# Kernel tuning notes

Hardware: AMD Instinct MI355X
Metric: run time of the kernel (lower is better)

The kernel has to match this reference:

```python
import jax, jax.numpy as jnp
import numpy as np

NP_, NT_, D_, E_, EP_, L_, R_ = 100000, 300000, 64, 2000000, 500000, 2, 2


def setup_inputs() -> dict:
    key = jax.random.key(0)
    ks = jax.random.split(key, 12)
    return {
        "emb_playlist": jax.random.normal(ks[0], (NP_, D_), jnp.float32),
        "emb_track": jax.random.normal(ks[1], (NT_, D_), jnp.float32),
        "W_rel": jax.random.normal(ks[2], (L_, R_, D_, D_), jnp.float32) * 0.1,
        "W_root": jax.random.normal(ks[3], (L_, D_, D_), jnp.float32) * 0.1,
        "bias": jnp.zeros((L_, D_), jnp.float32),
        "n_id_playlist": jnp.arange(NP_, dtype=jnp.int32),
        "n_id_track": jnp.arange(NT_, dtype=jnp.int32),
        "edge_pt_src": jax.random.randint(ks[4], (E_,), 0, NP_, jnp.int32),
        "edge_pt_dst": jax.random.randint(ks[5], (E_,), 0, NT_, jnp.int32),
        "edge_tp_src": jax.random.randint(ks[6], (E_,), 0, NT_, jnp.int32),
        "edge_tp_dst": jax.random.randint(ks[7], (E_,), 0, NP_, jnp.int32),
        "ell_pl": jax.random.randint(ks[8], (EP_,), 0, NP_, jnp.int32),
        "ell_tr": jax.random.randint(ks[9], (EP_,), 0, NT_, jnp.int32),
    }


def _hetero_gnn(emb_playlist, emb_track, W_rel, W_root, bias,
                n_id_playlist, n_id_track,
                edge_pt_src, edge_pt_dst, edge_tp_src, edge_tp_dst,
                ell_pl, ell_tr):
    NP = emb_playlist.shape[0]
    NT = emb_track.shape[0]
    L = W_root.shape[0]
    N = NP + NT

    # embedding lookup by n_id (identity here, but faithful gather)
    x_pl = emb_playlist[n_id_playlist]
    x_tr = emb_track[n_id_track]

    # alpha=None -> uniform 1/(L+1); buffer is softmaxed -> still uniform
    weights = jax.nn.softmax(jnp.full((L + 1,), 1.0 / (L + 1), jnp.float32))

    out_pl = x_pl * weights[0]
    out_tr = x_tr * weights[0]

    # homogeneous layout: playlists at [0, NP), tracks at [NP, NP+NT)
    x = jnp.concatenate([x_pl, x_tr], axis=0)
    rel_edges = [
        (edge_pt_src, edge_pt_dst + NP),   # playlist -> track
        (edge_tp_src + NP, edge_tp_dst),   # track -> playlist
    ]

    for i in range(L):
        # RGCNConv: root transform + per-relation mean aggregation
        h = x @ W_root[i] + bias[i]
        for r, (src, dst) in enumerate(rel_edges):
            hr = x @ W_rel[i, r]              # [N, D] transform-then-gather
            msg = hr[src]                     # [E, D]
            ssum = jax.ops.segment_sum(msg, dst, num_segments=N)
            cnt = jax.ops.segment_sum(jnp.ones_like(dst, dtype=x.dtype), dst,
                                      num_segments=N)
            h = h + ssum / jnp.maximum(cnt, 1.0)[:, None]
        x = jax.nn.relu(h)
        out_pl = out_pl + x[:NP] * weights[i + 1]
        out_tr = out_tr + x[NP:] * weights[i + 1]

    # global -> local mapping via searchsorted (faithful happy path)
    ps_idx = jnp.argsort(n_id_playlist)
    ps = n_id_playlist[ps_idx]
    pl_loc = ps_idx[jnp.clip(jnp.searchsorted(ps, ell_pl), 0, NP - 1)]
    ts_idx = jnp.argsort(n_id_track)
    ts = n_id_track[ts_idx]
    tr_loc = ts_idx[jnp.clip(jnp.searchsorted(ts, ell_tr), 0, NT - 1)]

    # dot-product link scores (dropout p=0.0 -> identity)
    return jnp.sum(out_pl[pl_loc] * out_tr[tr_loc], axis=-1)


def reference(emb_playlist, emb_track, W_rel, W_root, bias,
              n_id_playlist, n_id_track,
              edge_pt_src, edge_pt_dst, edge_tp_src, edge_tp_dst,
              ell_pl, ell_tr):
    return _hetero_gnn(emb_playlist, emb_track, W_rel, W_root, bias,
                       n_id_playlist, n_id_track,
                       edge_pt_src, edge_pt_dst, edge_tp_src, edge_tp_dst,
                       ell_pl, ell_tr)
```

## Files before the change

kernel.cpp:

```cpp
#include <hip/hip_runtime.h>
#include <stdint.h>

typedef __attribute__((ext_vector_type(8))) short bf16x8;
typedef __attribute__((ext_vector_type(4))) float f32x4;

#define BN 1024
#define BNSHIFT 10
#define MAXNB 512
#define PTI 8192
#define PTHREADS 512
#define EPT (PTI / PTHREADS)

static __device__ __forceinline__ float b2f_lo(uint32_t w) {
  union { uint32_t u; float f; } c; c.u = w << 16; return c.f;
}
static __device__ __forceinline__ float b2f_hi(uint32_t w) {
  union { uint32_t u; float f; } c; c.u = w & 0xffff0000u; return c.f;
}
static __device__ __forceinline__ uint16_t f2b(float f) {
  union { float f; uint32_t u; } c; c.f = f;
  return (uint16_t)((c.u + 0x7fffu + ((c.u >> 16) & 1u)) >> 16);
}
static __device__ __forceinline__ f32x4 unpack4(uint2 t) {
  f32x4 r;
  r.x = b2f_lo(t.x); r.y = b2f_hi(t.x);
  r.z = b2f_lo(t.y); r.w = b2f_hi(t.y);
  return r;
}
static __device__ __forceinline__ void acc8(float* s, uint4 v) {
  s[0] += b2f_lo(v.x); s[1] += b2f_hi(v.x);
  s[2] += b2f_lo(v.y); s[3] += b2f_hi(v.y);
  s[4] += b2f_lo(v.z); s[5] += b2f_hi(v.z);
  s[6] += b2f_lo(v.w); s[7] += b2f_hi(v.w);
}

__global__ __launch_bounds__(256) void convert_kernel(
    const float* __restrict__ emb_pl, const float* __restrict__ emb_tr,
    uint16_t* __restrict__ xb, int NP, int N) {
  long g = (long)blockIdx.x * 256 + threadIdx.x;
  long base8 = g * 8;
  long total = (long)N * 64;
  if (base8 >= total) return;
  long plEnd = (long)NP * 64;
  const float* src = (base8 < plEnd) ? (emb_pl + base8) : (emb_tr + (base8 - plEnd));
  f32x4 a = *(const f32x4*)src;
  f32x4 b = *(const f32x4*)(src + 4);
  union { uint16_t h[8]; uint4 v; } o;
  o.h[0] = f2b(a.x); o.h[1] = f2b(a.y); o.h[2] = f2b(a.z); o.h[3] = f2b(a.w);
  o.h[4] = f2b(b.x); o.h[5] = f2b(b.y); o.h[6] = f2b(b.z); o.h[7] = f2b(b.w);
  *(uint4*)(xb + base8) = o.v;
}

__global__ __launch_bounds__(256) void bucket_hist_kernel(
    const int* __restrict__ pt_dst, const int* __restrict__ tp_dst,
    int* __restrict__ bucketCount, int E, int NP, int NB) {
  extern __shared__ int hist[];
  int t = threadIdx.x;
  for (int b = t; b < NB; b += 256) hist[b] = 0;
  __syncthreads();
  long total = 2L * E;
  long stride = (long)gridDim.x * 256;
  for (long e = (long)blockIdx.x * 256 + t; e < total; e += stride) {
    int dstG = (e < E) ? (NP + pt_dst[e]) : tp_dst[e - E];
    atomicAdd(&hist[dstG >> BNSHIFT], 1);
  }
  __syncthreads();
  for (int b = t; b < NB; b += 256) {
    int h = hist[b];
    if (h > 0) atomicAdd(&bucketCount[b], h);
  }
}

__global__ __launch_bounds__(1024) void bucket_scan_kernel(
    const int* __restrict__ bucketCount, int* __restrict__ bucketStart,
    int* __restrict__ gCursor, int NB) {
  __shared__ int s[1024];
  int t = threadIdx.x;
  int K = (NB + 1023) >> 10;
  int b0 = t * K;
  int local = 0;
  for (int j = 0; j < K; ++j) {
    int b = b0 + j;
    if (b < NB) local += bucketCount[b];
  }
  int acc = local;
  s[t] = local;
  __syncthreads();
  for (int off = 1; off < 1024; off <<= 1) {
    int u = (t >= off) ? s[t - off] : 0;
    __syncthreads();
    acc += u;
    s[t] = acc;
    __syncthreads();
  }
  int run = acc - local;
  for (int j = 0; j < K; ++j) {
    int b = b0 + j;
    if (b < NB) {
      bucketStart[b] = run;
      gCursor[b] = run;
      run += bucketCount[b];
    }
  }
}

__global__ __launch_bounds__(PTHREADS) void partition_kernel(
    const int* __restrict__ pt_src, const int* __restrict__ pt_dst,
    const int* __restrict__ tp_src, const int* __restrict__ tp_dst,
    int* __restrict__ gCursor, uint32_t* __restrict__ pk,
    int E, int NP, int NB) {
  __shared__ uint64_t buf[PTI];
  __shared__ int hist[MAXNB];
  __shared__ int lstart[MAXNB];
  __shared__ int gbase[MAXNB];
  __shared__ int cur[MAXNB];
  __shared__ int sc[PTHREADS];
  int t = threadIdx.x;
  long total = 2L * E;
  long e0 = (long)blockIdx.x * PTI;
  long rem = total - e0;
  int cnt = (rem < (long)PTI) ? (int)rem : PTI;

  for (int j = t; j < NB; j += PTHREADS) hist[j] = 0;
  __syncthreads();

  int bj[EPT];
  uint32_t pkj[EPT];
#pragma unroll
  for (int j = 0; j < EPT; ++j) {
    int i = j * PTHREADS + t;
    bj[j] = -1;
    if (i < cnt) {
      long e = e0 + i;
      int dstG, src;
      if (e < E) {
        dstG = NP + pt_dst[e];
        src = pt_src[e];
      } else {
        dstG = tp_dst[e - E];
        src = NP + tp_src[e - E];
      }
      int b = dstG >> BNSHIFT;
      bj[j] = b;
      pkj[j] = ((uint32_t)(dstG & (BN - 1)) << 20) | (uint32_t)src;
      atomicAdd(&hist[b], 1);
    }
  }
  __syncthreads();

  int h = (t < NB) ? hist[t] : 0;
  int acc = h;
  sc[t] = h;
  __syncthreads();
  for (int off = 1; off < PTHREADS; off <<= 1) {
    int u = (t >= off) ? sc[t - off] : 0;
    __syncthreads();
    acc += u;
    sc[t] = acc;
    __syncthreads();
  }
  if (t < NB) {
    int ls = acc - h;
    lstart[t] = ls;
    cur[t] = ls;
    gbase[t] = (h > 0) ? atomicAdd(&gCursor[t], h) : 0;
  }
  __syncthreads();

#pragma unroll
  for (int j = 0; j < EPT; ++j) {
    int b = bj[j];
    if (b >= 0) {
      int pos = atomicAdd(&cur[b], 1);
      int gpos = gbase[b] + (pos - lstart[b]);
      buf[pos] = ((uint64_t)(uint32_t)gpos << 32) | (uint64_t)pkj[j];
    }
  }
  __syncthreads();

  for (int i = t; i < cnt; i += PTHREADS) {
    uint64_t e = buf[i];
    pk[(uint32_t)(e >> 32)] = (uint32_t)e;
  }
}

__global__ __launch_bounds__(512) void local_csr_kernel(
    const int* __restrict__ bucketStart, const int* __restrict__ bucketCount,
    const uint32_t* __restrict__ pk, int* __restrict__ rowptr,
    int* __restrict__ col, int N, int TEtotal) {
  __shared__ int hist[BN];
  __shared__ int cur[BN];
  __shared__ int ssum[512];
  int t = threadIdx.x;
  int b = blockIdx.x;
  hist[t] = 0;
  hist[t + 512] = 0;
  __syncthreads();
  int beg = bucketStart[b], num = bucketCount[b];
  for (int i = t; i < num; i += 512)
    atomicAdd(&hist[pk[beg + i] >> 20], 1);
  __syncthreads();
  int base0 = t * 2;
  int h0 = hist[base0], h1 = hist[base0 + 1];
  int tot = h0 + h1;
  int acc = tot;
  ssum[t] = tot;
  __syncthreads();
  for (int off = 1; off < 512; off <<= 1) {
    int u = (t >= off) ? ssum[t - off] : 0;
    __syncthreads();
    acc += u;
    ssum[t] = acc;
    __syncthreads();
  }
  int run = acc - tot;
  int ex0 = run, ex1 = run + h0;
  cur[base0] = ex0;
  cur[base0 + 1] = ex1;
  int node0 = (b << BNSHIFT) + base0;
  if (node0 < N) rowptr[node0] = beg + ex0;
  if (node0 + 1 < N) rowptr[node0 + 1] = beg + ex1;
  __syncthreads();
  for (int i = t; i < num; i += 512) {
    uint32_t w = pk[beg + i];
    int dl = (int)(w >> 20);
    int pos = atomicAdd(&cur[dl], 1);
    col[beg + pos] = (int)(w & 0xFFFFFu);
  }
  if (b == 0 && t == 0) rowptr[N] = TEtotal;
}

__global__ __launch_bounds__(256) void pull_kernel(
    const int* __restrict__ rowptr, const int* __restrict__ col,
    const uint16_t* __restrict__ base, uint16_t* __restrict__ agg, int N) {
  int node = blockIdx.x * 32 + (threadIdx.x >> 3);
  int c = threadIdx.x & 7;
  if (node >= N) return;
  int beg = rowptr[node], end = rowptr[node + 1];
  float s[8] = {0, 0, 0, 0, 0, 0, 0, 0};
  const uint16_t* bp = base + c * 8;
  int i = beg;
  for (; i + 4 <= end; i += 4) {
    int c0 = col[i], c1 = col[i + 1], c2 = col[i + 2], c3 = col[i + 3];
    uint4 v0 = *(const uint4*)(bp + (size_t)c0 * 64);
    uint4 v1 = *(const uint4*)(bp + (size_t)c1 * 64);
    uint4 v2 = *(const uint4*)(bp + (size_t)c2 * 64);
    uint4 v3 = *(const uint4*)(bp + (size_t)c3 * 64);
    acc8(s, v0); acc8(s, v1); acc8(s, v2); acc8(s, v3);
  }
  for (; i < end; ++i)
    acc8(s, *(const uint4*)(bp + (size_t)col[i] * 64));
  int deg = end - beg;
  float inv = 1.0f / (float)(deg > 1 ? deg : 1);
  union { uint16_t h[8]; uint4 v; } o;
#pragma unroll
  for (int j = 0; j < 8; ++j) o.h[j] = f2b(s[j] * inv);
  *(uint4*)(agg + (size_t)node * 64 + c * 8) = o.v;
}

__global__ __launch_bounds__(256) void transform_kernel(
    const uint16_t* __restrict__ xpl, const uint16_t* __restrict__ xtr,
    const uint16_t* __restrict__ agg,
    const float* __restrict__ Wroot,
    const float* __restrict__ WrelP, const float* __restrict__ WrelT,
    const float* __restrict__ biasrow,
    uint16_t* __restrict__ xout, int NP, int NT, int BP) {
  int wave = threadIdx.x >> 6;
  int lane = threadIdx.x & 63;
  int m = lane & 15, q = lane >> 4;

  int wl, nw, ntiles, nodeBase;
  const uint16_t* xbase;
  const float* Wrel;
  if ((int)blockIdx.x < BP) {
    wl = blockIdx.x * 4 + wave; nw = BP * 4; ntiles = NP / 16;
    xbase = xpl; Wrel = WrelP; nodeBase = 0;
  } else {
    wl = (blockIdx.x - BP) * 4 + wave; nw = (gridDim.x - BP) * 4; ntiles = NT / 16;
    xbase = xtr; Wrel = WrelT; nodeBase = NP;
  }

  bf16x8 br[2][4], bl[2][4];
  for (int kc = 0; kc < 2; ++kc)
    for (int ct = 0; ct < 4; ++ct) {
      int n = 16 * ct + m;
      int k0 = 32 * kc + 8 * q;
      bf16x8 t0, t1;
      for (int i = 0; i < 8; ++i) {
        t0[i] = (short)f2b(Wroot[(size_t)(k0 + i) * 64 + n]);
        t1[i] = (short)f2b(Wrel[(size_t)(k0 + i) * 64 + n]);
      }
      br[kc][ct] = t0;
      bl[kc][ct] = t1;
    }
  float bv[4];
  for (int ct = 0; ct < 4; ++ct) bv[ct] = biasrow[16 * ct + m];

  for (int t = wl; t < ntiles; t += nw) {
    int rowLocal = t * 16 + m;
    int nodeG = nodeBase + rowLocal;
    const uint16_t* xrow = xbase + (size_t)rowLocal * 64;
    bf16x8 ax0 = *(const bf16x8*)(xrow + 8 * q);
    bf16x8 ax1 = *(const bf16x8*)(xrow + 32 + 8 * q);

    const uint16_t* arow = agg + (size_t)nodeG * 64;
    bf16x8 aa0 = *(const bf16x8*)(arow + 8 * q);
    bf16x8 aa1 = *(const bf16x8*)(arow + 32 + 8 * q);

    f32x4 acc[4];
#pragma unroll
    for (int ct = 0; ct < 4; ++ct) acc[ct] = (f32x4){bv[ct], bv[ct], bv[ct], bv[ct]};
#pragma unroll
    for (int ct = 0; ct < 4; ++ct) {
      acc[ct] = __builtin_amdgcn_mfma_f32_16x16x32_bf16(ax0, br[0][ct], acc[ct], 0, 0, 0);
      acc[ct] = __builtin_amdgcn_mfma_f32_16x16x32_bf16(ax1, br[1][ct], acc[ct], 0, 0, 0);
      acc[ct] = __builtin_amdgcn_mfma_f32_16x16x32_bf16(aa0, bl[0][ct], acc[ct], 0, 0, 0);
      acc[ct] = __builtin_amdgcn_mfma_f32_16x16x32_bf16(aa1, bl[1][ct], acc[ct], 0, 0, 0);
    }
    int nodeRow0 = nodeBase + t * 16;
#pragma unroll
    for (int ct = 0; ct < 4; ++ct)
#pragma unroll
      for (int r = 0; r < 4; ++r) {
        float v = acc[ct][r];
        v = v > 0.0f ? v : 0.0f;
        xout[(size_t)(nodeRow0 + 4 * q + r) * 64 + 16 * ct + m] = f2b(v);
      }
  }
}

__global__ __launch_bounds__(256) void sum_kernel(
    const float* __restrict__ emb_pl, const float* __restrict__ emb_tr,
    const uint16_t* __restrict__ x1, const uint16_t* __restrict__ x2,
    uint16_t* __restrict__ S, int NP, int N) {
  long g = (long)blockIdx.x * 256 + threadIdx.x;
  long b8 = g * 8;
  long total = (long)N * 64;
  if (b8 >= total) return;
  long plEnd = (long)NP * 64;
  const float* e = (b8 < plEnd) ? (emb_pl + b8) : (emb_tr + (b8 - plEnd));
  f32x4 ea = *(const f32x4*)e;
  f32x4 eb = *(const f32x4*)(e + 4);
  uint4 x1v = *(const uint4*)(x1 + b8);
  uint4 x2v = *(const uint4*)(x2 + b8);
  f32x4 fa1 = unpack4(make_uint2(x1v.x, x1v.y)), fb1 = unpack4(make_uint2(x1v.z, x1v.w));
  f32x4 fa2 = unpack4(make_uint2(x2v.x, x2v.y)), fb2 = unpack4(make_uint2(x2v.z, x2v.w));
  union { uint16_t h[8]; uint4 v; } o;
  o.h[0] = f2b(ea.x + fa1.x + fa2.x);
  o.h[1] = f2b(ea.y + fa1.y + fa2.y);
  o.h[2] = f2b(ea.z + fa1.z + fa2.z);
  o.h[3] = f2b(ea.w + fa1.w + fa2.w);
  o.h[4] = f2b(eb.x + fb1.x + fb2.x);
  o.h[5] = f2b(eb.y + fb1.y + fb2.y);
  o.h[6] = f2b(eb.z + fb1.z + fb2.z);
  o.h[7] = f2b(eb.w + fb1.w + fb2.w);
  *(uint4*)(S + b8) = o.v;
}

__global__ void score_kernel(const int* __restrict__ ell_pl,
                             const int* __restrict__ ell_tr,
                             const uint16_t* __restrict__ S,
                             float* __restrict__ out, int EP, int NP) {
  long g = (long)blockIdx.x * blockDim.x + threadIdx.x;
  long pair = g >> 3;
  int c = (int)(g & 7);
  if (pair >= EP) return;
  int p = ell_pl[pair];
  int t = ell_tr[pair];
  uint4 vp = *(const uint4*)(S + (size_t)p * 64 + c * 8);
  uint4 vt = *(const uint4*)(S + (size_t)(NP + t) * 64 + c * 8);
  float partial = b2f_lo(vp.x) * b2f_lo(vt.x) + b2f_hi(vp.x) * b2f_hi(vt.x)
                + b2f_lo(vp.y) * b2f_lo(vt.y) + b2f_hi(vp.y) * b2f_hi(vt.y)
                + b2f_lo(vp.z) * b2f_lo(vt.z) + b2f_hi(vp.z) * b2f_hi(vt.z)
                + b2f_lo(vp.w) * b2f_lo(vt.w) + b2f_hi(vp.w) * b2f_hi(vt.w);
  partial += __shfl_xor(partial, 1);
  partial += __shfl_xor(partial, 2);
  partial += __shfl_xor(partial, 4);
  if (c == 0) out[pair] = partial * (1.0f / 9.0f);
}

extern "C" void kernel_launch(void* const* d_in, const int* in_sizes, int n_in,
                              void* d_out, int out_size, void* d_ws, size_t ws_size,
                              hipStream_t stream) {
  const float* emb_pl = (const float*)d_in[0];
  const float* emb_tr = (const float*)d_in[1];
  const float* W_rel = (const float*)d_in[2];
  const float* W_root = (const float*)d_in[3];
  const float* bias = (const float*)d_in[4];
  const int* pt_src = (const int*)d_in[7];
  const int* pt_dst = (const int*)d_in[8];
  const int* tp_src = (const int*)d_in[9];
  const int* tp_dst = (const int*)d_in[10];
  const int* ell_pl = (const int*)d_in[11];
  const int* ell_tr = (const int*)d_in[12];
  float* out = (float*)d_out;

  const int NP = in_sizes[5];
  const int NT = in_sizes[6];
  const int E = in_sizes[7];
  const int EP = in_sizes[11];
  const int N = NP + NT;
  const long TE = 2L * E;
  const int NB = (N + BN - 1) / BN;

  char* ws = (char*)d_ws;
  size_t off = 0;
  uint16_t* agg = (uint16_t*)(ws + off); off += (size_t)N * 64 * 2;
  uint16_t* x1  = (uint16_t*)(ws + off); off += (size_t)N * 64 * 2;
  uint16_t* x2  = (uint16_t*)(ws + off); off += (size_t)N * 64 * 2;
  uint32_t* pk  = (uint32_t*)(ws + off); off += (size_t)TE * 4;
  int* col      = (int*)(ws + off);      off += (size_t)TE * 4;
  int* rowptr   = (int*)(ws + off);      off += (size_t)(N + 1) * 4;
  int* bucketCount = (int*)(ws + off);   off += (size_t)NB * 4;
  int* bucketStart = (int*)(ws + off);   off += (size_t)NB * 4;
  int* gCursor     = (int*)(ws + off);   off += (size_t)NB * 4;

  uint16_t* xb0 = x2;
  uint16_t* S = agg;

  const int TB = 256;
  long cvt = ((long)N * 64 / 8 + TB - 1) / TB;
  int pullBlocks = (N + 31) / 32;
  int scoreBlocks = (int)(((long)EP * 8 + TB - 1) / TB);
  int partBlocks = (int)((TE + PTI - 1) / PTI);
  const int BP = 256, GT = 1024;

  convert_kernel<<<(int)cvt, TB, 0, stream>>>(emb_pl, emb_tr, xb0, NP, N);

  hipMemsetAsync(bucketCount, 0, (size_t)NB * 4, stream);
  bucket_hist_kernel<<<128, TB, NB * 4, stream>>>(pt_dst, tp_dst, bucketCount,
                                                  E, NP, NB);
  bucket_scan_kernel<<<1, 1024, 0, stream>>>(bucketCount, bucketStart, gCursor, NB);
  partition_kernel<<<partBlocks, PTHREADS, 0, stream>>>(
      pt_src, pt_dst, tp_src, tp_dst, gCursor, pk, E, NP, NB);
  local_csr_kernel<<<NB, 512, 0, stream>>>(bucketStart, bucketCount, pk,
                                           rowptr, col, N, (int)TE);

  pull_kernel<<<pullBlocks, TB, 0, stream>>>(rowptr, col, xb0, agg, N);
  transform_kernel<<<GT, TB, 0, stream>>>(
      xb0, xb0 + (size_t)NP * 64, agg, W_root + 0 * 4096, W_rel + 1 * 4096,
      W_rel + 0 * 4096, bias + 0, x1, NP, NT, BP);

  pull_kernel<<<pullBlocks, TB, 0, stream>>>(rowptr, col, x1, agg, N);
  transform_kernel<<<GT, TB, 0, stream>>>(
      x1, x1 + (size_t)NP * 64, agg, W_root + 1 * 4096, W_rel + 3 * 4096,
      W_rel + 2 * 4096, bias + 64, x2, NP, NT, BP);

  sum_kernel<<<(int)cvt, TB, 0, stream>>>(emb_pl, emb_tr, x1, x2, S, NP, N);
  score_kernel<<<scoreBlocks, TB, 0, stream>>>(ell_pl, ell_tr, S, out, EP, NP);
}
```

Measured before the change: 554.1 us.

## Fuse final layer-sum into second transform, add nontemporal loads and deeper pull unroll

Removes the separate sum_kernel: the second transform now adds the fp32 embedding and layer-1 output to its ReLU result and writes the summed score input S directly, saving a full pass over N×64 data and one launch. Streaming loads and stores across most kernels are marked nontemporal so they bypass cache retention. The pull kernel gets an 8-wide unrolled gather loop to keep more loads in flight. The fused epilogue does scalar, per-element reads of emb and x1, which may be poorly coalesced, and S aliases agg, which the same kernel reads.

After: 606.3 us. +9.4%, slower.

```diff
diff --git a/kernel.cpp b/kernel.cpp
--- a/kernel.cpp
+++ b/kernel.cpp
@@ -3,6 +3,7 @@
 
 typedef __attribute__((ext_vector_type(8))) short bf16x8;
 typedef __attribute__((ext_vector_type(4))) float f32x4;
+typedef __attribute__((ext_vector_type(4))) uint32_t u32x4;
 
 #define BN 1024
 #define BNSHIFT 10
@@ -43,8 +44,8 @@
   if (base8 >= total) return;
   long plEnd = (long)NP * 64;
   const float* src = (base8 < plEnd) ? (emb_pl + base8) : (emb_tr + (base8 - plEnd));
-  f32x4 a = *(const f32x4*)src;
-  f32x4 b = *(const f32x4*)(src + 4);
+  f32x4 a = __builtin_nontemporal_load((const f32x4*)src);
+  f32x4 b = __builtin_nontemporal_load((const f32x4*)(src + 4));
   union { uint16_t h[8]; uint4 v; } o;
   o.h[0] = f2b(a.x); o.h[1] = f2b(a.y); o.h[2] = f2b(a.z); o.h[3] = f2b(a.w);
   o.h[4] = f2b(b.x); o.h[5] = f2b(b.y); o.h[6] = f2b(b.z); o.h[7] = f2b(b.w);
@@ -61,7 +62,8 @@
   long total = 2L * E;
   long stride = (long)gridDim.x * 256;
   for (long e = (long)blockIdx.x * 256 + t; e < total; e += stride) {
-    int dstG = (e < E) ? (NP + pt_dst[e]) : tp_dst[e - E];
+    int dstG = (e < E) ? (NP + __builtin_nontemporal_load(&pt_dst[e]))
+                       : __builtin_nontemporal_load(&tp_dst[e - E]);
     atomicAdd(&hist[dstG >> BNSHIFT], 1);
   }
   __syncthreads();
@@ -134,11 +136,11 @@
       long e = e0 + i;
       int dstG, src;
       if (e < E) {
-        dstG = NP + pt_dst[e];
-        src = pt_src[e];
+        dstG = NP + __builtin_nontemporal_load(&pt_dst[e]);
+        src = __builtin_nontemporal_load(&pt_src[e]);
       } else {
-        dstG = tp_dst[e - E];
-        src = NP + tp_src[e - E];
+        dstG = __builtin_nontemporal_load(&tp_dst[e - E]);
+        src = NP + __builtin_nontemporal_load(&tp_src[e - E]);
       }
       int b = dstG >> BNSHIFT;
       bj[j] = b;
@@ -198,7 +200,7 @@
   __syncthreads();
   int beg = bucketStart[b], num = bucketCount[b];
   for (int i = t; i < num; i += 512)
-    atomicAdd(&hist[pk[beg + i] >> 20], 1);
+    atomicAdd(&hist[__builtin_nontemporal_load(&pk[beg + i]) >> 20], 1);
   __syncthreads();
   int base0 = t * 2;
   int h0 = hist[base0], h1 = hist[base0 + 1];
@@ -222,7 +224,7 @@
   if (node0 + 1 < N) rowptr[node0 + 1] = beg + ex1;
   __syncthreads();
   for (int i = t; i < num; i += 512) {
-    uint32_t w = pk[beg + i];
+    uint32_t w = __builtin_nontemporal_load(&pk[beg + i]);
     int dl = (int)(w >> 20);
     int pos = atomicAdd(&cur[dl], 1);
     col[beg + pos] = (int)(w & 0xFFFFFu);
@@ -240,8 +242,21 @@
   float s[8] = {0, 0, 0, 0, 0, 0, 0, 0};
   const uint16_t* bp = base + c * 8;
   int i = beg;
+  for (; i + 8 <= end; i += 8) {
+    int cc[8];
+#pragma unroll
+    for (int j = 0; j < 8; ++j) cc[j] = __builtin_nontemporal_load(&col[i + j]);
+    uint4 v[8];
+#pragma unroll
+    for (int j = 0; j < 8; ++j) v[j] = *(const uint4*)(bp + (size_t)cc[j] * 64);
+#pragma unroll
+    for (int j = 0; j < 8; ++j) acc8(s, v[j]);
+  }
   for (; i + 4 <= end; i += 4) {
-    int c0 = col[i], c1 = col[i + 1], c2 = col[i + 2], c3 = col[i + 3];
+    int c0 = __builtin_nontemporal_load(&col[i]);
+    int c1 = __builtin_nontemporal_load(&col[i + 1]);
+    int c2 = __builtin_nontemporal_load(&col[i + 2]);
+    int c3 = __builtin_nontemporal_load(&col[i + 3]);
     uint4 v0 = *(const uint4*)(bp + (size_t)c0 * 64);
     uint4 v1 = *(const uint4*)(bp + (size_t)c1 * 64);
     uint4 v2 = *(const uint4*)(bp + (size_t)c2 * 64);
@@ -249,21 +264,23 @@
     acc8(s, v0); acc8(s, v1); acc8(s, v2); acc8(s, v3);
   }
   for (; i < end; ++i)
-    acc8(s, *(const uint4*)(bp + (size_t)col[i] * 64));
+    acc8(s, *(const uint4*)(bp + (size_t)__builtin_nontemporal_load(&col[i]) * 64));
   int deg = end - beg;
   float inv = 1.0f / (float)(deg > 1 ? deg : 1);
-  union { uint16_t h[8]; uint4 v; } o;
+  union { uint16_t h[8]; u32x4 v; } o;
 #pragma unroll
   for (int j = 0; j < 8; ++j) o.h[j] = f2b(s[j] * inv);
-  *(uint4*)(agg + (size_t)node * 64 + c * 8) = o.v;
-}
-
+  __builtin_nontemporal_store(o.v, (u32x4*)(agg + (size_t)node * 64 + c * 8));
+}
+
+template <bool FUSE>
 __global__ __launch_bounds__(256) void transform_kernel(
     const uint16_t* __restrict__ xpl, const uint16_t* __restrict__ xtr,
     const uint16_t* __restrict__ agg,
     const float* __restrict__ Wroot,
     const float* __restrict__ WrelP, const float* __restrict__ WrelT,
     const float* __restrict__ biasrow,
+    const float* __restrict__ embP, const float* __restrict__ embT,
     uint16_t* __restrict__ xout, int NP, int NT, int BP) {
   int wave = threadIdx.x >> 6;
   int lane = threadIdx.x & 63;
@@ -272,12 +289,13 @@
   int wl, nw, ntiles, nodeBase;
   const uint16_t* xbase;
   const float* Wrel;
+  const float* embBase;
   if ((int)blockIdx.x < BP) {
     wl = blockIdx.x * 4 + wave; nw = BP * 4; ntiles = NP / 16;
-    xbase = xpl; Wrel = WrelP; nodeBase = 0;
+    xbase = xpl; Wrel = WrelP; nodeBase = 0; embBase = embP;
   } else {
     wl = (blockIdx.x - BP) * 4 + wave; nw = (gridDim.x - BP) * 4; ntiles = NT / 16;
-    xbase = xtr; Wrel = WrelT; nodeBase = NP;
+    xbase = xtr; Wrel = WrelT; nodeBase = NP; embBase = embT;
   }
 
   bf16x8 br[2][4], bl[2][4];
@@ -300,12 +318,18 @@
     int rowLocal = t * 16 + m;
     int nodeG = nodeBase + rowLocal;
     const uint16_t* xrow = xbase + (size_t)rowLocal * 64;
-    bf16x8 ax0 = *(const bf16x8*)(xrow + 8 * q);
-    bf16x8 ax1 = *(const bf16x8*)(xrow + 32 + 8 * q);
+    bf16x8 ax0, ax1;
+    if (FUSE) {
+      ax0 = *(const bf16x8*)(xrow + 8 * q);
+      ax1 = *(const bf16x8*)(xrow + 32 + 8 * q);
+    } else {
+      ax0 = __builtin_nontemporal_load((const bf16x8*)(xrow + 8 * q));
+      ax1 = __builtin_nontemporal_load((const bf16x8*)(xrow + 32 + 8 * q));
+    }
 
     const uint16_t* arow = agg + (size_t)nodeG * 64;
-    bf16x8 aa0 = *(const bf16x8*)(arow + 8 * q);
-    bf16x8 aa1 = *(const bf16x8*)(arow + 32 + 8 * q);
+    bf16x8 aa0 = __builtin_nontemporal_load((const bf16x8*)(arow + 8 * q));
+    bf16x8 aa1 = __builtin_nontemporal_load((const bf16x8*)(arow + 32 + 8 * q));
 
     f32x4 acc[4];
 #pragma unroll
@@ -318,43 +342,25 @@
       acc[ct] = __builtin_amdgcn_mfma_f32_16x16x32_bf16(aa1, bl[1][ct], acc[ct], 0, 0, 0);
     }
     int nodeRow0 = nodeBase + t * 16;
+    int localRow0 = t * 16;
 #pragma unroll
     for (int ct = 0; ct < 4; ++ct)
 #pragma unroll
       for (int r = 0; r < 4; ++r) {
         float v = acc[ct][r];
         v = v > 0.0f ? v : 0.0f;
-        xout[(size_t)(nodeRow0 + 4 * q + r) * 64 + 16 * ct + m] = f2b(v);
+        int colIdx = 16 * ct + m;
+        size_t go = (size_t)(nodeRow0 + 4 * q + r) * 64 + colIdx;
+        if (FUSE) {
+          size_t lo = (size_t)(localRow0 + 4 * q + r) * 64 + colIdx;
+          float e = __builtin_nontemporal_load(&embBase[lo]);
+          float x1f = b2f_lo((uint32_t)xbase[lo]);
+          xout[go] = f2b(e + x1f + v);
+        } else {
+          xout[go] = f2b(v);
+        }
       }
   }
-}
-
-__global__ __launch_bounds__(256) void sum_kernel(
-    const float* __restrict__ emb_pl, const float* __restrict__ emb_tr,
-    const uint16_t* __restrict__ x1, const uint16_t* __restrict__ x2,
-    uint16_t* __restrict__ S, int NP, int N) {
-  long g = (long)blockIdx.x * 256 + threadIdx.x;
-  long b8 = g * 8;
-  long total = (long)N * 64;
-  if (b8 >= total) return;
-  long plEnd = (long)NP * 64;
-  const float* e = (b8 < plEnd) ? (emb_pl + b8) : (emb_tr + (b8 - plEnd));
-  f32x4 ea = *(const f32x4*)e;
-  f32x4 eb = *(const f32x4*)(e + 4);
-  uint4 x1v = *(const uint4*)(x1 + b8);
-  uint4 x2v = *(const uint4*)(x2 + b8);
-  f32x4 fa1 = unpack4(make_uint2(x1v.x, x1v.y)), fb1 = unpack4(make_uint2(x1v.z, x1v.w));
-  f32x4 fa2 = unpack4(make_uint2(x2v.x, x2v.y)), fb2 = unpack4(make_uint2(x2v.z, x2v.w));
-  union { uint16_t h[8]; uint4 v; } o;
-  o.h[0] = f2b(ea.x + fa1.x + fa2.x);
-  o.h[1] = f2b(ea.y + fa1.y + fa2.y);
-  o.h[2] = f2b(ea.z + fa1.z + fa2.z);
-  o.h[3] = f2b(ea.w + fa1.w + fa2.w);
-  o.h[4] = f2b(eb.x + fb1.x + fb2.x);
-  o.h[5] = f2b(eb.y + fb1.y + fb2.y);
-  o.h[6] = f2b(eb.z + fb1.z + fb2.z);
-  o.h[7] = f2b(eb.w + fb1.w + fb2.w);
-  *(uint4*)(S + b8) = o.v;
 }
 
 __global__ void score_kernel(const int* __restrict__ ell_pl,
@@ -365,8 +371,8 @@
   long pair = g >> 3;
   int c = (int)(g & 7);
   if (pair >= EP) return;
-  int p = ell_pl[pair];
-  int t = ell_tr[pair];
+  int p = __builtin_nontemporal_load(&ell_pl[pair]);
+  int t = __builtin_nontemporal_load(&ell_tr[pair]);
   uint4 vp = *(const uint4*)(S + (size_t)p * 64 + c * 8);
   uint4 vt = *(const uint4*)(S + (size_t)(NP + t) * 64 + c * 8);
   float partial = b2f_lo(vp.x) * b2f_lo(vt.x) + b2f_hi(vp.x) * b2f_hi(vt.x)
@@ -376,7 +382,7 @@
   partial += __shfl_xor(partial, 1);
   partial += __shfl_xor(partial, 2);
   partial += __shfl_xor(partial, 4);
-  if (c == 0) out[pair] = partial * (1.0f / 9.0f);
+  if (c == 0) __builtin_nontemporal_store(partial * (1.0f / 9.0f), &out[pair]);
 }
 
 extern "C" void kernel_launch(void* const* d_in, const int* in_sizes, int n_in,
@@ -407,7 +413,7 @@
   size_t off = 0;
   uint16_t* agg = (uint16_t*)(ws + off); off += (size_t)N * 64 * 2;
   uint16_t* x1  = (uint16_t*)(ws + off); off += (size_t)N * 64 * 2;
-  uint16_t* x2  = (uint16_t*)(ws + off); off += (size_t)N * 64 * 2;
+  uint16_t* xb0 = (uint16_t*)(ws + off); off += (size_t)N * 64 * 2;
   uint32_t* pk  = (uint32_t*)(ws + off); off += (size_t)TE * 4;
   int* col      = (int*)(ws + off);      off += (size_t)TE * 4;
   int* rowptr   = (int*)(ws + off);      off += (size_t)(N + 1) * 4;
@@ -415,7 +421,6 @@
   int* bucketStart = (int*)(ws + off);   off += (size_t)NB * 4;
   int* gCursor     = (int*)(ws + off);   off += (size_t)NB * 4;
 
-  uint16_t* xb0 = x2;
   uint16_t* S = agg;
 
   const int TB = 256;
@@ -437,15 +442,14 @@
                                            rowptr, col, N, (int)TE);
 
   pull_kernel<<<pullBlocks, TB, 0, stream>>>(rowptr, col, xb0, agg, N);
-  transform_kernel<<<GT, TB, 0, stream>>>(
+  transform_kernel<false><<<GT, TB, 0, stream>>>(
       xb0, xb0 + (size_t)NP * 64, agg, W_root + 0 * 4096, W_rel + 1 * 4096,
-      W_rel + 0 * 4096, bias + 0, x1, NP, NT, BP);
+      W_rel + 0 * 4096, bias + 0, nullptr, nullptr, x1, NP, NT, BP);
 
   pull_kernel<<<pullBlocks, TB, 0, stream>>>(rowptr, col, x1, agg, N);
-  transform_kernel<<<GT, TB, 0, stream>>>(
+  transform_kernel<true><<<GT, TB, 0, stream>>>(
       x1, x1 + (size_t)NP * 64, agg, W_root + 1 * 4096, W_rel + 3 * 4096,
-      W_rel + 2 * 4096, bias + 64, x2, NP, NT, BP);
-
-  sum_kernel<<<(int)cvt, TB, 0, stream>>>(emb_pl, emb_tr, x1, x2, S, NP, N);
+      W_rel + 2 * 4096, bias + 64, emb_pl, emb_tr, S, NP, NT, BP);
+
   score_kernel<<<scoreBlocks, TB, 0, stream>>>(ell_pl, ell_tr, S, out, EP, NP);
 }
```
